# Optimization experiments

Measured on AMD Instinct MI355X. Metric: run time of the kernel, lower is better.

The kernel has to match this reference:

```python
import jax, jax.numpy as jnp
import numpy as np
from jax import lax

D = 1024
H = 1024


def setup_inputs() -> dict:
    key = jax.random.key(0)
    ks = jax.random.split(key, 6)
    N, T = 256, 64
    x = jax.random.normal(ks[0], (N, T, D), dtype=jnp.float32)
    A = jax.random.normal(ks[1], (N, H, 4, 4), dtype=jnp.float32)
    Wx = jax.random.normal(ks[2], (D, 4 * H), dtype=jnp.float32) / np.sqrt(D)
    Wh = jax.random.normal(ks[3], (H, 4 * H), dtype=jnp.float32) / np.sqrt(H)
    Wattn = jax.random.normal(ks[4], (H, 4 * H), dtype=jnp.float32) / np.sqrt(H)
    b = jnp.zeros((4 * H,), dtype=jnp.float32)
    return {"x": x, "A": A, "Wx": Wx, "Wh": Wh, "Wattn": Wattn, "b": b}


def reference(x, A, Wx, Wh, Wattn, b):
    N, T, Din = x.shape
    Hh = A.shape[1]
    A_flat = A.reshape(N, Hh, -1)  # (N, H, 16)
    inv_sqrt_h = jnp.asarray(1.0 / np.sqrt(Hh), dtype=x.dtype)
    h0 = jnp.mean(A, axis=(2, 3))  # (N, H)
    c0 = h0

    def step(carry, xt):
        prev_h, prev_c = carry
        # dot-product attention over the 16 spatial positions
        scores = jnp.einsum('nh,nhp->np', prev_h, A_flat) * inv_sqrt_h
        w = jax.nn.softmax(scores, axis=-1)          # (N, 16)
        attn = jnp.einsum('nhp,np->nh', A_flat, w)   # (N, H)
        # fused LSTM gate preactivation
        a = xt @ Wx + prev_h @ Wh + attn @ Wattn + b  # (N, 4H)
        i, f, o, g = jnp.split(a, 4, axis=-1)
        next_c = jax.nn.sigmoid(f) * prev_c + jax.nn.sigmoid(i) * jnp.tanh(g)
        next_h = jax.nn.sigmoid(o) * jnp.tanh(next_c)
        return (next_h, next_c), next_h

    _, hs = lax.scan(step, (h0, c0), jnp.swapaxes(x, 0, 1))  # hs: (T, N, H)
    return jnp.swapaxes(hs, 0, 1)  # (N, T, H)
```

## Files before the change

kernel.cpp:

```cpp
#include <hip/hip_runtime.h>

typedef __bf16 bf16;
typedef bf16 bf16x8 __attribute__((ext_vector_type(8)));
typedef bf16 bf16x4 __attribute__((ext_vector_type(4)));
typedef float f32x4 __attribute__((ext_vector_type(4)));

#define NB 256
#define TS 64
#define DD 1024
#define HH 1024
#define NOUT 4096


static __device__ __forceinline__ void gload_lds16(const void* g, void* l) {
  __builtin_amdgcn_global_load_lds(
      (const __attribute__((address_space(1))) void*)g,
      (__attribute__((address_space(3))) void*)l, 16, 0, 0);
}

#define SWZ_ADD(v, imm) \
  (v) += __int_as_float(__builtin_amdgcn_ds_swizzle(__float_as_int(v), imm))
#define SWZ_MAX(v, imm) \
  (v) = fmaxf(v, __int_as_float(__builtin_amdgcn_ds_swizzle(__float_as_int(v), imm)))

__global__ __launch_bounds__(256) void convert_bf(const float* __restrict__ in,
                                                  bf16* __restrict__ o) {
  const size_t gid = (size_t)blockIdx.x * 256 + threadIdx.x;
  bf16x8 v;
#pragma unroll
  for (int j = 0; j < 8; ++j) v[j] = (bf16)in[gid * 8 + j];
  *(bf16x8*)(o + gid * 8) = v;
}

__global__ __launch_bounds__(256) void convert_wt(const float* __restrict__ W,
                                                  bf16* __restrict__ Wt) {
  const int gid = blockIdx.x * 256 + threadIdx.x;
  const int tile = gid >> 6, l = gid & 63;
  const int tau = tile >> 5, kt = tile & 31;
  const int cx = tau * 16 + (l & 15);
  const int ht = cx >> 6, rem = cx & 63;
  const int co = (rem & 3) * HH + ht * 16 + (rem >> 2);
  const int k0 = kt * 32 + (l >> 4) * 8;
  bf16x8 o;
#pragma unroll
  for (int j = 0; j < 8; ++j) o[j] = (bf16)W[(size_t)(k0 + j) * NOUT + co];
  *(bf16x8*)(Wt + (size_t)tile * 512 + l * 8) = o;
}

__global__ __launch_bounds__(1024) void transpose_A(const float* __restrict__ A,
                                                    bf16* __restrict__ At) {
  __shared__ float lt[1024 * 17];
  const int n = blockIdx.x, u = threadIdx.x;
  const float* ar = A + ((size_t)n * HH + u) * 16;
#pragma unroll
  for (int q = 0; q < 4; ++q) {
    f32x4 v = *(const f32x4*)(ar + q * 4);
#pragma unroll
    for (int r = 0; r < 4; ++r) lt[u * 17 + q * 4 + r] = v[r];
  }
  __syncthreads();
  const int p = u >> 6, seg = u & 63;
  bf16x8 o0, o1;
#pragma unroll
  for (int j = 0; j < 8; ++j) {
    o0[j] = (bf16)lt[(seg * 16 + j) * 17 + p];
    o1[j] = (bf16)lt[(seg * 16 + 8 + j) * 17 + p];
  }
  bf16* dst = At + (size_t)(n * 16 + p) * 1024 + seg * 16;
  *(bf16x8*)dst = o0;
  *(bf16x8*)(dst + 8) = o1;
}

template <int MODE>
__global__ __launch_bounds__(256, 3) void gemm128(const bf16* __restrict__ Am,
                                                  const bf16* __restrict__ Bt,
                                                  bf16* __restrict__ C) {
  __shared__ __align__(16) bf16 astg[2][8 * 512];
  __shared__ __align__(16) bf16 bstg[2][8 * 512];
  const int b = blockIdx.x;
  const int ct = (b & 7) * 4 + ((b >> 3) & 3);
  const int rt = b >> 5;
  const int tid = threadIdx.x, lane = tid & 63, wid = tid >> 6;
  const int wr = wid >> 1, wc = wid & 1;

  const bf16* gA[2];
  const bf16* gB[2];
  int lA[2], lB[2];
#pragma unroll
  for (int e = 0; e < 2; ++e) {
    const int mt = wid * 2 + e;
    gA[e] = Am + (size_t)(rt * 128 + mt * 16 + (lane & 15)) * 1024 + (lane >> 4) * 8;
    lA[e] = mt * 512;
    gB[e] = Bt + ((size_t)(ct * 8 + mt) * 32) * 512 + lane * 8;
    lB[e] = mt * 512;
  }
  f32x4 acc[4][4];
#pragma unroll
  for (int i = 0; i < 4; ++i)
#pragma unroll
    for (int j = 0; j < 4; ++j) acc[i][j] = (f32x4){0, 0, 0, 0};

#pragma unroll
  for (int e = 0; e < 2; ++e) {
    gload_lds16(gA[e], &astg[0][lA[e]]);
    gload_lds16(gB[e], &bstg[0][lB[e]]);
  }
  for (int it = 0; it < 32; ++it) {
    __syncthreads();
    if (it < 31) {
#pragma unroll
      for (int e = 0; e < 2; ++e) {
        gload_lds16(gA[e] + (it + 1) * 32, &astg[(it + 1) & 1][lA[e]]);
        gload_lds16(gB[e] + (size_t)(it + 1) * 512, &bstg[(it + 1) & 1][lB[e]]);
      }
    }
    const bf16* ab = astg[it & 1];
    const bf16* bb = bstg[it & 1];
    bf16x8 af[4], bfr[4];
#pragma unroll
    for (int i = 0; i < 4; ++i) af[i] = *(const bf16x8*)(ab + (wr * 4 + i) * 512 + lane * 8);
#pragma unroll
    for (int j = 0; j < 4; ++j) bfr[j] = *(const bf16x8*)(bb + (wc * 4 + j) * 512 + lane * 8);
#pragma unroll
    for (int i = 0; i < 4; ++i)
#pragma unroll
      for (int j = 0; j < 4; ++j)
        acc[i][j] = __builtin_amdgcn_mfma_f32_16x16x32_bf16(af[i], bfr[j], acc[i][j], 0, 0, 0);
  }
#pragma unroll
  for (int i = 0; i < 4; ++i)
#pragma unroll
    for (int j = 0; j < 4; ++j) {
      const int row0 = rt * 128 + wr * 64 + i * 16 + (lane >> 4) * 4;
      const int col = ct * 128 + wc * 64 + j * 16 + (lane & 15);
#pragma unroll
      for (int r = 0; r < 4; ++r) {
        const int row = row0 + r;
        size_t idx;
        if (MODE == 0) idx = ((size_t)(row & 63) * NB + (row >> 6)) * NOUT + col;
        else           idx = (size_t)(row >> 4) * (NOUT * 16) + (size_t)col * 16 + (row & 15);
        C[idx] = (bf16)acc[i][j][r];
      }
    }
}

__global__ __launch_bounds__(1024) void init_kernel(const float* __restrict__ A,
                                                    float* __restrict__ c_ws,
                                                    bf16* __restrict__ Aop0,
                                                    float* __restrict__ s0) {
  __shared__ float h_sh[1024];
  __shared__ float scA[16], scB[16];
  const int n = (blockIdx.x & 7) * 32 + (blockIdx.x >> 3);
  const int u = threadIdx.x;
  const float* arow = A + ((size_t)n * HH + u) * 16;
  float h0 = 0.f;
#pragma unroll
  for (int p = 0; p < 16; ++p) h0 += arow[p];
  h0 *= 0.0625f;
  c_ws[(n << 10) + u] = h0;
  h_sh[u] = h0;
  Aop0[(n << 10) + u] = (bf16)h0;
  __syncthreads();
  const int lane = u & 63, w = u >> 6;
  const float* ap = A + (size_t)n * (HH * 16) + w;
  float s = 0.f;
#pragma unroll
  for (int i = 0; i < 16; ++i) {
    const int idx = lane + 64 * i;
    s = fmaf(h_sh[idx], ap[(size_t)idx * 16], s);
  }
  SWZ_ADD(s, 0x041F); SWZ_ADD(s, 0x081F); SWZ_ADD(s, 0x101F);
  SWZ_ADD(s, 0x201F); SWZ_ADD(s, 0x401F);
  if (lane == 0) scA[w] = s;
  else if (lane == 32) scB[w] = s;
  __syncthreads();
  if (u < 16) s0[n * 16 + u] = scA[u] + scB[u];
}

#define STEP_SMEM 65536
__global__ __launch_bounds__(512, 4) void step_kernel(
    const bf16* __restrict__ Aop_cur, bf16* __restrict__ Aop_nxt,
    const bf16* __restrict__ Wh_t, const bf16* __restrict__ xWx2,
    const bf16* __restrict__ G2, const float* __restrict__ s_cur,
    float* __restrict__ s_nxt, float* __restrict__ s_zro,
    const float* __restrict__ bias, const bf16* __restrict__ A_bf,
    float* __restrict__ c_ws, float* __restrict__ out, const int t) {
  __shared__ __align__(16) char smem[STEP_SMEM];
  __shared__ float w_sh[512];
  bf16* astg = (bf16*)smem;
  float* red = (float*)smem;

  const int b = blockIdx.x;
  const int xcd = b & 7;
  const int ht = xcd * 8 + ((b >> 3) & 7);
  const int rt = b >> 6;
  const int tid = threadIdx.x, lane = tid & 63, wid = tid >> 6;
  const int kg = wid >> 1, ow = wid & 1;
  const int nloc = tid >> 4, hl = tid & 15;
  const int n = rt * 32 + nloc, h = ht * 16 + hl;

  float ss = s_cur[n * 16 + hl];

#pragma unroll
  for (int e = 0; e < 8; ++e) {
    const int tau = wid * 8 + e;
    const int tkg = tau >> 4, tmt = (tau >> 3) & 1, tks = tau & 7;
    const bf16* src = Aop_cur +
        (size_t)(rt * 32 + tmt * 16 + (lane & 15)) * 1024 +
        tkg * 256 + tks * 32 + (lane >> 4) * 8;
    gload_lds16(src, astg + tkg * 8192 + (tmt * 8 + tks) * 512);
  }

  bf16x8 gq[8];
  {
    const bf16* Gp = G2 + (size_t)n * (NOUT * 16) + (size_t)(ht * 64 + hl * 4) * 16;
#pragma unroll
    for (int e = 0; e < 8; ++e) gq[e] = *(const bf16x8*)(Gp + e * 8);
  }
  const bf16x4 xv = *(const bf16x4*)(xWx2 + (size_t)t * (NB * NOUT) +
                                     (size_t)n * NOUT + ht * 64 + hl * 4);
  if (tid < 8) s_zro[b * 8 + tid] = 0.f;

  {
    ss *= 0.03125f;
    float m = ss;
    SWZ_MAX(m, 0x041F); SWZ_MAX(m, 0x081F); SWZ_MAX(m, 0x101F); SWZ_MAX(m, 0x201F);
    const float e = expf(ss - m);
    float su = e;
    SWZ_ADD(su, 0x041F); SWZ_ADD(su, 0x081F); SWZ_ADD(su, 0x101F); SWZ_ADD(su, 0x201F);
    w_sh[tid] = e / su;
  }
  __syncthreads();

  const bf16* gB0 = Wh_t + ((size_t)(ht * 4 + ow * 2 + 0) * 32 + kg * 8) * 512 + lane * 8;
  const bf16* gB1 = Wh_t + ((size_t)(ht * 4 + ow * 2 + 1) * 32 + kg * 8) * 512 + lane * 8;
  f32x4 a00 = {0, 0, 0, 0}, a01 = {0, 0, 0, 0}, a10 = {0, 0, 0, 0}, a11 = {0, 0, 0, 0};
  {
    const bf16* ab = astg + kg * 8192;
    bf16x8 bc0 = *(const bf16x8*)gB0;
    bf16x8 bc1 = *(const bf16x8*)gB1;
    __builtin_amdgcn_s_setprio(1);
#pragma unroll
    for (int ks = 0; ks < 8; ++ks) {
      bf16x8 bn0, bn1;
      if (ks < 7) {
        bn0 = *(const bf16x8*)(gB0 + (ks + 1) * 512);
        bn1 = *(const bf16x8*)(gB1 + (ks + 1) * 512);
      }
      const bf16x8 f0 = *(const bf16x8*)(ab + ks * 512 + lane * 8);
      const bf16x8 f1 = *(const bf16x8*)(ab + (8 + ks) * 512 + lane * 8);
      a00 = __builtin_amdgcn_mfma_f32_16x16x32_bf16(f0, bc0, a00, 0, 0, 0);
      a01 = __builtin_amdgcn_mfma_f32_16x16x32_bf16(f0, bc1, a01, 0, 0, 0);
      a10 = __builtin_amdgcn_mfma_f32_16x16x32_bf16(f1, bc0, a10, 0, 0, 0);
      a11 = __builtin_amdgcn_mfma_f32_16x16x32_bf16(f1, bc1, a11, 0, 0, 0);
      if (ks < 7) { bc0 = bn0; bc1 = bn1; }
    }
    __builtin_amdgcn_s_setprio(0);
  }
  __syncthreads();

  {
    const int cb = kg * 64 + ow * 32 + (lane & 15);
    const int nb = (lane >> 4) * 4;
    *(f32x4*)&red[(cb)*36 + nb] = a00;
    *(f32x4*)&red[(cb + 16) * 36 + nb] = a01;
    *(f32x4*)&red[(cb)*36 + nb + 16] = a10;
    *(f32x4*)&red[(cb + 16) * 36 + nb + 16] = a11;
  }
  __syncthreads();

  f32x4 gv = {0, 0, 0, 0};
#pragma unroll
  for (int k2 = 0; k2 < 4; ++k2)
#pragma unroll
    for (int g = 0; g < 4; ++g) gv[g] += red[(k2 * 64 + hl * 4 + g) * 36 + nloc];
#pragma unroll
  for (int g = 0; g < 4; ++g) {
    float acc = 0.f;
#pragma unroll
    for (int p = 0; p < 8; ++p) acc = fmaf(w_sh[nloc * 16 + p], (float)gq[g * 2][p], acc);
#pragma unroll
    for (int p = 0; p < 8; ++p) acc = fmaf(w_sh[nloc * 16 + 8 + p], (float)gq[g * 2 + 1][p], acc);
    gv[g] += acc;
  }
  const float ai = gv[0] + (float)xv[0] + bias[h];
  const float af = gv[1] + (float)xv[1] + bias[HH + h];
  const float ao = gv[2] + (float)xv[2] + bias[2 * HH + h];
  const float ag = gv[3] + (float)xv[3] + bias[3 * HH + h];
  const float cold = c_ws[(n << 10) + h];
  const float si = 1.f / (1.f + expf(-ai));
  const float sf = 1.f / (1.f + expf(-af));
  const float so = 1.f / (1.f + expf(-ao));
  const float cn = sf * cold + si * tanhf(ag);
  const float hn = so * tanhf(cn);
  c_ws[(n << 10) + h] = cn;
  out[((size_t)n * TS + t) * HH + h] = hn;
  Aop_nxt[(n << 10) + h] = (bf16)hn;

  if (t < TS - 1) {
    __syncthreads();
    const bf16* arow = A_bf + ((size_t)n * HH + h) * 16;
    const bf16x8 av0 = *(const bf16x8*)arow;
    const bf16x8 av1 = *(const bf16x8*)(arow + 8);
#pragma unroll
    for (int r = 0; r < 8; ++r) {
      red[(nloc * 16 + r) * 17 + hl] = hn * (float)av0[r];
      red[(nloc * 16 + 8 + r) * 17 + hl] = hn * (float)av1[r];
    }
    __syncthreads();
    const float* r2 = &red[(nloc * 16 + hl) * 17];
    float s = 0.f;
#pragma unroll
    for (int q = 0; q < 16; ++q) s += r2[q];
    atomicAdd(&s_nxt[n * 16 + hl], s);
  }
}

extern "C" void kernel_launch(void* const* d_in, const int* in_sizes, int n_in,
                              void* d_out, int out_size, void* d_ws, size_t ws_size,
                              hipStream_t stream) {
  const float* x     = (const float*)d_in[0];
  const float* A     = (const float*)d_in[1];
  const float* Wx    = (const float*)d_in[2];
  const float* Wh    = (const float*)d_in[3];
  const float* Wattn = (const float*)d_in[4];
  const float* bias  = (const float*)d_in[5];
  float* out = (float*)d_out;
  char* ws = (char*)d_ws;
  bf16* Wh_t   = (bf16*)(ws + 0);
  bf16* Wat_t  = (bf16*)(ws + 8388608);
  bf16* At     = (bf16*)(ws + 16777216);
  bf16* A_bf   = (bf16*)(ws + 25165824);
  bf16* xWx2   = (bf16*)(ws + 33554432);
  bf16* G2     = (bf16*)(ws + 167772160);
  bf16* x_bf   = (bf16*)(ws + 201326592);
  bf16* Wxt    = (bf16*)(ws + 234881024);
  bf16* Aop0   = (bf16*)(ws + 243269632);
  bf16* Aop1   = (bf16*)(ws + 243793920);
  float* s0    = (float*)(ws + 244318208);
  float* s1    = (float*)(ws + 244334592);
  float* s2    = (float*)(ws + 244350976);
  float* c_ws  = (float*)(ws + 244367360);

  hipMemsetAsync(s1, 0, 16384, stream);
  convert_bf<<<8192, 256, 0, stream>>>(x, x_bf);
  convert_bf<<<2048, 256, 0, stream>>>(A, A_bf);
  convert_wt<<<2048, 256, 0, stream>>>(Wx, Wxt);
  convert_wt<<<2048, 256, 0, stream>>>(Wh, Wh_t);
  convert_wt<<<2048, 256, 0, stream>>>(Wattn, Wat_t);
  gemm128<0><<<4096, 256, 0, stream>>>(x_bf, Wxt, xWx2);
  transpose_A<<<256, 1024, 0, stream>>>(A, At);
  gemm128<1><<<1024, 256, 0, stream>>>(At, Wat_t, G2);
  init_kernel<<<256, 1024, 0, stream>>>(A, c_ws, Aop0, s0);
  for (int t = 0; t < TS; ++t) {
    float* scur = (t % 3 == 0) ? s0 : (t % 3 == 1) ? s1 : s2;
    float* snxt = (t % 3 == 0) ? s1 : (t % 3 == 1) ? s2 : s0;
    float* szro = (t % 3 == 0) ? s2 : (t % 3 == 1) ? s0 : s1;
    step_kernel<<<512, 512, 0, stream>>>((t & 1) ? Aop1 : Aop0,
                                         (t & 1) ? Aop0 : Aop1, Wh_t, xWx2, G2,
                                         scur, snxt, szro, bias, A_bf, c_ws,
                                         out, t);
  }
}
```

Baseline: 1.404 ms.

## Halve step-kernel batch tile, fold bias into xWx GEMM, remap GEMM block order

Each step kernel now covers 16 batch rows instead of 32, using 256 threads and 1024 blocks, so each block needs half the shared memory and the grid fills more CUs. Each wave now computes four output column tiles from a single A fragment. The bias add moves out of the per-step loop into the epilogue of the input-projection GEMM. The GEMM block-to-tile mapping changes per mode to improve L2 locality across XCDs. The trade-off is that Wh is streamed twice as often across blocks, since each block still reads the full Wh slice for its columns.

```diff
diff --git a/kernel.cpp b/kernel.cpp
--- a/kernel.cpp
+++ b/kernel.cpp
@@ -74,12 +74,14 @@
 template <int MODE>
 __global__ __launch_bounds__(256, 3) void gemm128(const bf16* __restrict__ Am,
                                                   const bf16* __restrict__ Bt,
-                                                  bf16* __restrict__ C) {
+                                                  bf16* __restrict__ C,
+                                                  const float* __restrict__ bias) {
   __shared__ __align__(16) bf16 astg[2][8 * 512];
   __shared__ __align__(16) bf16 bstg[2][8 * 512];
   const int b = blockIdx.x;
-  const int ct = (b & 7) * 4 + ((b >> 3) & 3);
-  const int rt = b >> 5;
+  const int xcd = b & 7;
+  const int rt = (MODE == 0) ? (xcd * 16 + ((b >> 3) & 15)) : (xcd * 4 + ((b >> 3) & 3));
+  const int ct = (MODE == 0) ? (b >> 7) : (b >> 5);
   const int tid = threadIdx.x, lane = tid & 63, wid = tid >> 6;
   const int wr = wid >> 1, wc = wid & 1;
 
@@ -128,20 +130,26 @@
         acc[i][j] = __builtin_amdgcn_mfma_f32_16x16x32_bf16(af[i], bfr[j], acc[i][j], 0, 0, 0);
   }
 #pragma unroll
-  for (int i = 0; i < 4; ++i)
-#pragma unroll
-    for (int j = 0; j < 4; ++j) {
+  for (int j = 0; j < 4; ++j) {
+    const int col = ct * 128 + wc * 64 + j * 16 + (lane & 15);
+    float bv = 0.f;
+    if (MODE == 0) {
+      const int rem = col & 63;
+      bv = bias[(rem & 3) * HH + (col >> 6) * 16 + (rem >> 2)];
+    }
+#pragma unroll
+    for (int i = 0; i < 4; ++i) {
       const int row0 = rt * 128 + wr * 64 + i * 16 + (lane >> 4) * 4;
-      const int col = ct * 128 + wc * 64 + j * 16 + (lane & 15);
 #pragma unroll
       for (int r = 0; r < 4; ++r) {
         const int row = row0 + r;
         size_t idx;
         if (MODE == 0) idx = ((size_t)(row & 63) * NB + (row >> 6)) * NOUT + col;
         else           idx = (size_t)(row >> 4) * (NOUT * 16) + (size_t)col * 16 + (row & 15);
-        C[idx] = (bf16)acc[i][j][r];
+        C[idx] = (bf16)(acc[i][j][r] + bv);
       }
     }
+  }
 }
 
 __global__ __launch_bounds__(1024) void init_kernel(const float* __restrict__ A,
@@ -177,16 +185,16 @@
   if (u < 16) s0[n * 16 + u] = scA[u] + scB[u];
 }
 
-#define STEP_SMEM 65536
-__global__ __launch_bounds__(512, 4) void step_kernel(
+#define STEP_SMEM 32768
+__global__ __launch_bounds__(256, 4) void step_kernel(
     const bf16* __restrict__ Aop_cur, bf16* __restrict__ Aop_nxt,
     const bf16* __restrict__ Wh_t, const bf16* __restrict__ xWx2,
     const bf16* __restrict__ G2, const float* __restrict__ s_cur,
     float* __restrict__ s_nxt, float* __restrict__ s_zro,
-    const float* __restrict__ bias, const bf16* __restrict__ A_bf,
-    float* __restrict__ c_ws, float* __restrict__ out, const int t) {
+    const bf16* __restrict__ A_bf, float* __restrict__ c_ws,
+    float* __restrict__ out, const int t) {
   __shared__ __align__(16) char smem[STEP_SMEM];
-  __shared__ float w_sh[512];
+  __shared__ float w_sh[256];
   bf16* astg = (bf16*)smem;
   float* red = (float*)smem;
 
@@ -194,21 +202,18 @@
   const int xcd = b & 7;
   const int ht = xcd * 8 + ((b >> 3) & 7);
   const int rt = b >> 6;
-  const int tid = threadIdx.x, lane = tid & 63, wid = tid >> 6;
-  const int kg = wid >> 1, ow = wid & 1;
+  const int tid = threadIdx.x, lane = tid & 63, kg = tid >> 6;
   const int nloc = tid >> 4, hl = tid & 15;
-  const int n = rt * 32 + nloc, h = ht * 16 + hl;
+  const int n = rt * 16 + nloc, h = ht * 16 + hl;
 
   float ss = s_cur[n * 16 + hl];
 
 #pragma unroll
   for (int e = 0; e < 8; ++e) {
-    const int tau = wid * 8 + e;
-    const int tkg = tau >> 4, tmt = (tau >> 3) & 1, tks = tau & 7;
-    const bf16* src = Aop_cur +
-        (size_t)(rt * 32 + tmt * 16 + (lane & 15)) * 1024 +
-        tkg * 256 + tks * 32 + (lane >> 4) * 8;
-    gload_lds16(src, astg + tkg * 8192 + (tmt * 8 + tks) * 512);
+    const int tau = kg * 8 + e;
+    const bf16* src = Aop_cur + (size_t)(rt * 16 + (lane & 15)) * 1024 +
+                      tau * 32 + (lane >> 4) * 8;
+    gload_lds16(src, astg + tau * 512);
   }
 
   bf16x8 gq[8];
@@ -219,7 +224,7 @@
   }
   const bf16x4 xv = *(const bf16x4*)(xWx2 + (size_t)t * (NB * NOUT) +
                                      (size_t)n * NOUT + ht * 64 + hl * 4);
-  if (tid < 8) s_zro[b * 8 + tid] = 0.f;
+  if (tid < 4) s_zro[b * 4 + tid] = 0.f;
 
   {
     ss *= 0.03125f;
@@ -232,40 +237,41 @@
   }
   __syncthreads();
 
-  const bf16* gB0 = Wh_t + ((size_t)(ht * 4 + ow * 2 + 0) * 32 + kg * 8) * 512 + lane * 8;
-  const bf16* gB1 = Wh_t + ((size_t)(ht * 4 + ow * 2 + 1) * 32 + kg * 8) * 512 + lane * 8;
-  f32x4 a00 = {0, 0, 0, 0}, a01 = {0, 0, 0, 0}, a10 = {0, 0, 0, 0}, a11 = {0, 0, 0, 0};
+  const bf16* gB[4];
+#pragma unroll
+  for (int j = 0; j < 4; ++j)
+    gB[j] = Wh_t + ((size_t)(ht * 4 + j) * 32 + kg * 8) * 512 + lane * 8;
+  f32x4 acc[4];
+#pragma unroll
+  for (int j = 0; j < 4; ++j) acc[j] = (f32x4){0, 0, 0, 0};
   {
-    const bf16* ab = astg + kg * 8192;
-    bf16x8 bc0 = *(const bf16x8*)gB0;
-    bf16x8 bc1 = *(const bf16x8*)gB1;
+    bf16x8 bc[4], bn[4];
+#pragma unroll
+    for (int j = 0; j < 4; ++j) bc[j] = *(const bf16x8*)gB[j];
     __builtin_amdgcn_s_setprio(1);
 #pragma unroll
     for (int ks = 0; ks < 8; ++ks) {
-      bf16x8 bn0, bn1;
       if (ks < 7) {
-        bn0 = *(const bf16x8*)(gB0 + (ks + 1) * 512);
-        bn1 = *(const bf16x8*)(gB1 + (ks + 1) * 512);
+#pragma unroll
+        for (int j = 0; j < 4; ++j) bn[j] = *(const bf16x8*)(gB[j] + (ks + 1) * 512);
       }
-      const bf16x8 f0 = *(const bf16x8*)(ab + ks * 512 + lane * 8);
-      const bf16x8 f1 = *(const bf16x8*)(ab + (8 + ks) * 512 + lane * 8);
-      a00 = __builtin_amdgcn_mfma_f32_16x16x32_bf16(f0, bc0, a00, 0, 0, 0);
-      a01 = __builtin_amdgcn_mfma_f32_16x16x32_bf16(f0, bc1, a01, 0, 0, 0);
-      a10 = __builtin_amdgcn_mfma_f32_16x16x32_bf16(f1, bc0, a10, 0, 0, 0);
-      a11 = __builtin_amdgcn_mfma_f32_16x16x32_bf16(f1, bc1, a11, 0, 0, 0);
-      if (ks < 7) { bc0 = bn0; bc1 = bn1; }
+      const bf16x8 f0 = *(const bf16x8*)(astg + (kg * 8 + ks) * 512 + lane * 8);
+#pragma unroll
+      for (int j = 0; j < 4; ++j)
+        acc[j] = __builtin_amdgcn_mfma_f32_16x16x32_bf16(f0, bc[j], acc[j], 0, 0, 0);
+      if (ks < 7) {
+#pragma unroll
+        for (int j = 0; j < 4; ++j) bc[j] = bn[j];
+      }
     }
     __builtin_amdgcn_s_setprio(0);
   }
   __syncthreads();
 
-  {
-    const int cb = kg * 64 + ow * 32 + (lane & 15);
-    const int nb = (lane >> 4) * 4;
-    *(f32x4*)&red[(cb)*36 + nb] = a00;
-    *(f32x4*)&red[(cb + 16) * 36 + nb] = a01;
-    *(f32x4*)&red[(cb)*36 + nb + 16] = a10;
-    *(f32x4*)&red[(cb + 16) * 36 + nb + 16] = a11;
+#pragma unroll
+  for (int j = 0; j < 4; ++j) {
+    const int cb = kg * 64 + j * 16 + (lane & 15);
+    *(f32x4*)&red[cb * 20 + (lane >> 4) * 4] = acc[j];
   }
   __syncthreads();
 
@@ -273,20 +279,20 @@
 #pragma unroll
   for (int k2 = 0; k2 < 4; ++k2)
 #pragma unroll
-    for (int g = 0; g < 4; ++g) gv[g] += red[(k2 * 64 + hl * 4 + g) * 36 + nloc];
+    for (int g = 0; g < 4; ++g) gv[g] += red[(k2 * 64 + hl * 4 + g) * 20 + nloc];
 #pragma unroll
   for (int g = 0; g < 4; ++g) {
-    float acc = 0.f;
-#pragma unroll
-    for (int p = 0; p < 8; ++p) acc = fmaf(w_sh[nloc * 16 + p], (float)gq[g * 2][p], acc);
-#pragma unroll
-    for (int p = 0; p < 8; ++p) acc = fmaf(w_sh[nloc * 16 + 8 + p], (float)gq[g * 2 + 1][p], acc);
-    gv[g] += acc;
-  }
-  const float ai = gv[0] + (float)xv[0] + bias[h];
-  const float af = gv[1] + (float)xv[1] + bias[HH + h];
-  const float ao = gv[2] + (float)xv[2] + bias[2 * HH + h];
-  const float ag = gv[3] + (float)xv[3] + bias[3 * HH + h];
+    float a0 = 0.f;
+#pragma unroll
+    for (int p = 0; p < 8; ++p) a0 = fmaf(w_sh[nloc * 16 + p], (float)gq[g * 2][p], a0);
+#pragma unroll
+    for (int p = 0; p < 8; ++p) a0 = fmaf(w_sh[nloc * 16 + 8 + p], (float)gq[g * 2 + 1][p], a0);
+    gv[g] += a0;
+  }
+  const float ai = gv[0] + (float)xv[0];
+  const float af = gv[1] + (float)xv[1];
+  const float ao = gv[2] + (float)xv[2];
+  const float ag = gv[3] + (float)xv[3];
   const float cold = c_ws[(n << 10) + h];
   const float si = 1.f / (1.f + expf(-ai));
   const float sf = 1.f / (1.f + expf(-af));
@@ -348,17 +354,17 @@
   convert_wt<<<2048, 256, 0, stream>>>(Wx, Wxt);
   convert_wt<<<2048, 256, 0, stream>>>(Wh, Wh_t);
   convert_wt<<<2048, 256, 0, stream>>>(Wattn, Wat_t);
-  gemm128<0><<<4096, 256, 0, stream>>>(x_bf, Wxt, xWx2);
+  gemm128<0><<<4096, 256, 0, stream>>>(x_bf, Wxt, xWx2, bias);
   transpose_A<<<256, 1024, 0, stream>>>(A, At);
-  gemm128<1><<<1024, 256, 0, stream>>>(At, Wat_t, G2);
+  gemm128<1><<<1024, 256, 0, stream>>>(At, Wat_t, G2, nullptr);
   init_kernel<<<256, 1024, 0, stream>>>(A, c_ws, Aop0, s0);
   for (int t = 0; t < TS; ++t) {
     float* scur = (t % 3 == 0) ? s0 : (t % 3 == 1) ? s1 : s2;
     float* snxt = (t % 3 == 0) ? s1 : (t % 3 == 1) ? s2 : s0;
     float* szro = (t % 3 == 0) ? s2 : (t % 3 == 1) ? s0 : s1;
-    step_kernel<<<512, 512, 0, stream>>>((t & 1) ? Aop1 : Aop0,
-                                         (t & 1) ? Aop0 : Aop1, Wh_t, xWx2, G2,
-                                         scur, snxt, szro, bias, A_bf, c_ws,
-                                         out, t);
-  }
-}
+    step_kernel<<<1024, 256, 0, stream>>>((t & 1) ? Aop1 : Aop0,
+                                          (t & 1) ? Aop0 : Aop1, Wh_t, xWx2,
+                                          G2, scur, snxt, szro, A_bf, c_ws,
+                                          out, t);
+  }
+}
```

Result: slower. 1.449 ms (+3.2%).
